# Optimization experiments

Hardware: AMD Instinct MI355X
Metric: run time of the kernel (lower is better)

Reference implementation:

```python
import jax, jax.numpy as jnp
import numpy as np

S_REF = 2        # number of reference images
C = 1024         # DINOv3 ViT-L channel dim
H = W = 64       # 1024 / patch16 feature resolution
SVD = 500        # positional subspace rank


def _l2norm(x, axis):
    return x / jnp.clip(jnp.linalg.norm(x, axis=axis, keepdims=True), 1e-12)


def setup_inputs() -> dict:
    key = jax.random.key(0)
    k1, k2, k3 = jax.random.split(key, 3)
    fmaps = jax.random.normal(k1, (1, S_REF + 1, C, H, W), jnp.float32)
    ref_masks = jax.random.randint(k2, (S_REF, H, W), 0, 2) > 0  # bool masks at feature res
    basis_raw = jax.random.normal(k3, (C, SVD), jnp.float32)
    basis, _ = jnp.linalg.qr(basis_raw)  # orthonormal positional basis, as SVD U would be
    return {"fmaps": fmaps, "ref_masks": ref_masks, "basis": basis}


def reference(fmaps, ref_masks, basis):
    S = ref_masks.shape[0]
    B, T, Cc, h, w = fmaps.shape

    # F.normalize(fmaps, p=2, dim=2)
    fn = _l2norm(fmaps, 2)
    feat_tgt = fn[0, S]  # (C,h,w) raw-normalized target feats

    # _debias_features: project onto orthogonal complement of positional subspace.
    # (I - U U^T) X computed as X - U (U^T X) to avoid a CxC matrix.
    X = fn.reshape(B * T, Cc, h * w)
    coef = jnp.einsum('ck,bcn->bkn', basis, X)          # (BT, SVD, hw)
    Xd = X - jnp.einsum('ck,bkn->bcn', basis, coef)     # (BT, C, hw)
    fd = _l2norm(Xd.reshape(B, T, Cc, h, w), 2)
    feat_refs_deb = fd[0, :S]   # (S,C,h,w)
    feat_tgt_deb = fd[0, S]     # (C,h,w)

    # Masked feature pooling -> per-reference prototype, then averaged + renormalized
    maskf = ref_masks.astype(fn.dtype)                                  # (S,h,w)
    counts = jnp.clip(maskf.sum(axis=(1, 2)), 1.0)                      # guard empty mask
    protos = jnp.einsum('schw,shw->sc', feat_refs_deb, maskf) / counts[:, None]
    ref_prototype = _l2norm(protos.mean(axis=0), 0)                     # (C,)

    # Dense ref->target cosine-similarity maps: einsum 'bchw,bcxy->bhwxy'
    sim = jnp.einsum('schw,cxy->shwxy', feat_refs_deb, feat_tgt_deb)    # (S,h,w,h,w)

    # Forward matching: target-vs-prototype similarity
    sim_fwd = jnp.einsum('cxy,c->xy', feat_tgt_deb, ref_prototype)      # (h,w)

    # Backward matching votes: for each target patch, argmax over ref patches,
    # vote if the best ref patch lies inside the reference mask.
    sim_t2r = sim.transpose(0, 3, 4, 1, 2).reshape(S, h * w, h * w)     # (S, tgt, ref)
    best_idx = jnp.argmax(sim_t2r, axis=2)                              # (S, hw)
    mask_flat = ref_masks.reshape(S, h * w)
    votes = jnp.take_along_axis(mask_flat, best_idx, axis=1).astype(jnp.int32)
    votes = votes.sum(axis=0).reshape(h, w)                             # (h,w) int32

    return sim, sim_fwd, votes
```

## Files before the change

kernel.cpp:

```cpp
#include <hip/hip_runtime.h>
#include <hip/hip_bf16.h>
#include <cfloat>

#define CH   1024
#define HW   4096
#define NSVD 500
#define TFR  3
#define SREF 2

typedef __attribute__((ext_vector_type(4))) float f32x4;
typedef __attribute__((ext_vector_type(4))) unsigned int u32x4;
typedef __attribute__((ext_vector_type(8))) short short8;


__device__ inline unsigned bfr(float x) {
  unsigned u = __float_as_uint(x);
  return (u + 0x7fffu + ((u >> 16) & 1u)) >> 16;
}
__device__ inline float lores(float x, unsigned h) {
  return x - __uint_as_float(h << 16);
}
__device__ inline float vlo(unsigned ph, unsigned pl) {
  return __uint_as_float(ph << 16) + __uint_as_float(pl << 16);
}
__device__ inline float vhi(unsigned ph, unsigned pl) {
  return __uint_as_float(ph & 0xFFFF0000u) + __uint_as_float(pl & 0xFFFF0000u);
}

__global__ __launch_bounds__(256) void normpack_k(const float* __restrict__ src,
                                                  unsigned* __restrict__ Gh,
                                                  unsigned* __restrict__ Gl,
                                                  int fbase) {
  int t = blockIdx.x >> 6;
  int n0 = (blockIdx.x & 63) * 64;
  int tid = threadIdx.x, nl = tid & 63, r = tid >> 6;
  const float* base = src + (size_t)t * CH * HW + n0 + nl;
  float s = 0.f;
  for (int c = r; c < CH; c += 4) {
    float v = base[(size_t)c * HW];
    s += v * v;
  }
  __shared__ float red[256];
  __shared__ float inv[64];
  red[tid] = s;
  __syncthreads();
  if (r == 0)
    inv[nl] = 1.0f / fmaxf(sqrtf(red[nl] + red[nl + 64] + red[nl + 128] + red[nl + 192]), 1e-12f);
  __syncthreads();

  int cg = (tid & 15) * 4;
  int n4 = n0 + cg;
  float4 w4;
  w4.x = inv[cg]; w4.y = inv[cg + 1]; w4.z = inv[cg + 2]; w4.w = inv[cg + 3];
  int gt = fbase + t;
  for (int kg = tid >> 4; kg < 128; kg += 16) {
    const float* s0 = src + ((size_t)t * CH + kg * 8) * HW + n4;
    unsigned oh[4][4], ol[4][4];
#pragma unroll
    for (int j = 0; j < 4; j++) {
      float4 va = *reinterpret_cast<const float4*>(s0 + (size_t)(2 * j) * HW);
      float4 vb = *reinterpret_cast<const float4*>(s0 + (size_t)(2 * j + 1) * HW);
      float a[4] = {va.x * w4.x, va.y * w4.y, va.z * w4.z, va.w * w4.w};
      float b[4] = {vb.x * w4.x, vb.y * w4.y, vb.z * w4.z, vb.w * w4.w};
#pragma unroll
      for (int cc = 0; cc < 4; cc++) {
        unsigned ha = bfr(a[cc]), hb = bfr(b[cc]);
        oh[cc][j] = ha | (hb << 16);
        ol[cc][j] = bfr(lores(a[cc], ha)) | (bfr(lores(b[cc], hb)) << 16);
      }
    }
    size_t vib = (((size_t)gt * 16 + (n4 >> 8)) * 128 + kg) * 256 + (n4 & 255);
#pragma unroll
    for (int cc = 0; cc < 4; cc++) {
      *reinterpret_cast<u32x4*>(Gh + (vib + cc) * 4) = *reinterpret_cast<u32x4*>(oh[cc]);
      *reinterpret_cast<u32x4*>(Gl + (vib + cc) * 4) = *reinterpret_cast<u32x4*>(ol[cc]);
    }
  }
}

__global__ __launch_bounds__(256) void scale_pack_k(const float* __restrict__ src,
                                                    const float* __restrict__ inv,
                                                    unsigned* __restrict__ Gh,
                                                    unsigned* __restrict__ Gl) {
  int gid = blockIdx.x * 256 + threadIdx.x;
  int kg = gid >> 12;
  int n = gid & 4095;
  const float* s0 = src + (size_t)(kg * 8) * HW + n;
  float w = inv[n];
  unsigned oh[4], ol[4];
#pragma unroll
  for (int j = 0; j < 4; j++) {
    float a = s0[(size_t)(2 * j) * HW] * w;
    float b = s0[(size_t)(2 * j + 1) * HW] * w;
    unsigned ha = bfr(a), hb = bfr(b);
    oh[j] = ha | (hb << 16);
    ol[j] = bfr(lores(a, ha)) | (bfr(lores(b, hb)) << 16);
  }
  size_t vi = (((size_t)(n >> 8)) * 128 + kg) * 256 + (n & 255);
  *reinterpret_cast<u32x4*>(Gh + vi * 4) = *reinterpret_cast<u32x4*>(oh);
  *reinterpret_cast<u32x4*>(Gl + vi * 4) = *reinterpret_cast<u32x4*>(ol);
}

__global__ __launch_bounds__(256) void bt_k(const float* __restrict__ bas,
                                            float* __restrict__ bt) {
  int c0 = blockIdx.x * 64;
  __shared__ float tile[64][129];
  int tid = threadIdx.x;
  for (int kc = 0; kc < 512; kc += 128) {
    for (int cr = tid >> 7; cr < 64; cr += 2) {
      int k = kc + (tid & 127);
      tile[cr][tid & 127] = (k < NSVD) ? bas[(size_t)(c0 + cr) * NSVD + k] : 0.f;
    }
    __syncthreads();
    for (int kr = tid >> 6; kr < 128; kr += 4)
      bt[(size_t)(kc + kr) * 1024 + c0 + (tid & 63)] = tile[tid & 63][kr];
    __syncthreads();
  }
}

__global__ __launch_bounds__(256) void proj_pack_k(const float* __restrict__ bt,
                                                   unsigned* __restrict__ Ah,
                                                   unsigned* __restrict__ Al) {
  int m0 = blockIdx.x * 64, n0 = blockIdx.y * 64;
  int tid = threadIdx.x;
  int tx = tid & 15, ty = tid >> 4;
  int lm = tid & 63, lk = tid >> 6;
  __shared__ float As[16][64];
  __shared__ float Bs[16][64];
  float acc[4][4] = {};
  for (int k0 = 0; k0 < 512; k0 += 16) {
#pragma unroll
    for (int i = 0; i < 4; i++) {
      int k = k0 + lk * 4 + i;
      As[lk * 4 + i][lm] = bt[(size_t)k * 1024 + m0 + lm];
      Bs[lk * 4 + i][lm] = bt[(size_t)k * 1024 + n0 + lm];
    }
    __syncthreads();
#pragma unroll
    for (int kk = 0; kk < 16; kk++) {
      float a[4], b[4];
#pragma unroll
      for (int i = 0; i < 4; i++) a[i] = As[kk][ty * 4 + i];
#pragma unroll
      for (int j = 0; j < 4; j++) b[j] = Bs[kk][tx * 4 + j];
#pragma unroll
      for (int i = 0; i < 4; i++)
#pragma unroll
        for (int j = 0; j < 4; j++) acc[i][j] += a[i] * b[j];
    }
    __syncthreads();
  }
#pragma unroll
  for (int jp = 0; jp < 2; jp++) {
    int r = n0 / 2 + tx * 2 + jp;
#pragma unroll
    for (int i = 0; i < 4; i++) {
      int c = m0 + ty * 4 + i;
      float va = ((c == 2 * r) ? 1.0f : 0.0f) - acc[i][2 * jp];
      float vb = ((c == 2 * r + 1) ? 1.0f : 0.0f) - acc[i][2 * jp + 1];
      unsigned ha = bfr(va), hb = bfr(vb);
      size_t vi = ((size_t)((c >> 8) * 128 + (r >> 2)) * 256 + (c & 255)) * 4 + (r & 3);
      Ah[vi] = ha | (hb << 16);
      Al[vi] = bfr(lores(va, ha)) | (bfr(lores(vb, hb)) << 16);
    }
  }
}

__global__ __launch_bounds__(256) void pack_basis_k(const float* __restrict__ bas,
                                                    unsigned* __restrict__ Ah,
                                                    unsigned* __restrict__ Al) {
  int r = blockIdx.x;
  for (int m = threadIdx.x; m < 512; m += 256) {
    float b0 = (m < NSVD) ? bas[(size_t)(2 * r) * NSVD + m] : 0.f;
    float b1 = (m < NSVD) ? bas[(size_t)(2 * r + 1) * NSVD + m] : 0.f;
    unsigned h0 = bfr(b0), h1 = bfr(b1);
    int c = 1024 + m;
    size_t vi = ((size_t)((c >> 8) * 128 + (r >> 2)) * 256 + (c & 255)) * 4 + (r & 3);
    Ah[vi] = h0 | (h1 << 16);
    Al[vi] = bfr(lores(b0, h0)) | (bfr(lores(b1, h1)) << 16);
  }
}

__global__ __launch_bounds__(256) void inv2_k(const float* __restrict__ pbuf,
                                              float* __restrict__ invc) {
  int i = blockIdx.x * 256 + threadIdx.x;
  int s = i >> 12, n = i & 4095;
  float s2 = 0.f;
  if (s < 2) {
#pragma unroll
    for (int j = 0; j < 4; j++) s2 += pbuf[(size_t)(s * 8 + j) * HW + n];
    s2 = sqrtf(fmaxf(1.0f - s2, 0.0f));
  } else {
#pragma unroll
    for (int j = 16; j < 24; j++) s2 += pbuf[(size_t)j * HW + n];
    s2 = sqrtf(s2);
  }
  invc[i] = 1.0f / fmaxf(s2, 1e-12f);
}

__global__ __launch_bounds__(256) void proto_k(const unsigned* __restrict__ Gh,
                                               const unsigned* __restrict__ Gl,
                                               const int* __restrict__ mask,
                                               const float* __restrict__ invc,
                                               float* __restrict__ protos,
                                               float* __restrict__ counts) {
  int s = blockIdx.x >> 7, kg = blockIdx.x & 127;
  int tid = threadIdx.x;
  const u32x4* Hv = (const u32x4*)Gh + (size_t)s * 524288;
  const u32x4* Lv = (const u32x4*)Gl + (size_t)s * 524288;
  float a[8] = {};
  int cnt = 0;
  for (int n = tid; n < HW; n += 256) {
    if (mask[s * HW + n]) {
      cnt++;
      float w = invc[s * HW + n];
      size_t vi = ((size_t)(n >> 8) * 128 + kg) * 256 + (n & 255);
      u32x4 h = Hv[vi], l = Lv[vi];
#pragma unroll
      for (int j = 0; j < 4; j++) {
        a[2 * j] += vlo(h[j], l[j]) * w;
        a[2 * j + 1] += vhi(h[j], l[j]) * w;
      }
    }
  }
  __shared__ float red[256];
  for (int e = 0; e < 8; e++) {
    red[tid] = a[e];
    __syncthreads();
    for (int o = 128; o > 0; o >>= 1) {
      if (tid < o) red[tid] += red[tid + o];
      __syncthreads();
    }
    if (tid == 0) protos[s * CH + kg * 8 + e] = red[0];
    __syncthreads();
  }
  if (kg == 0) {
    red[tid] = (float)cnt;
    __syncthreads();
    for (int o = 128; o > 0; o >>= 1) {
      if (tid < o) red[tid] += red[tid + o];
      __syncthreads();
    }
    if (tid == 0) counts[s] = fmaxf(red[0], 1.0f);
  }
}

__global__ __launch_bounds__(256) void protomv_k(const unsigned* __restrict__ Ah,
                                                 const unsigned* __restrict__ Al,
                                                 const float* __restrict__ protos,
                                                 float* __restrict__ part) {
  int s = blockIdx.x >> 2;
  int c = (blockIdx.x & 3) * 256 + threadIdx.x;
  int kc = blockIdx.y;
  __shared__ float w[128];
  if (threadIdx.x < 128) w[threadIdx.x] = protos[s * CH + kc * 128 + threadIdx.x];
  __syncthreads();
  float acc = 0.f;
  for (int rl = 0; rl < 64; rl++) {
    int r = kc * 64 + rl;
    size_t vi = ((size_t)((c >> 8) * 128 + (r >> 2)) * 256 + (c & 255)) * 4 + (r & 3);
    unsigned h = Ah[vi], l = Al[vi];
    acc += vlo(h, l) * w[2 * rl] + vhi(h, l) * w[2 * rl + 1];
  }
  part[kc * 2048 + s * CH + c] = acc;
}

__global__ __launch_bounds__(256) void protonorm_k(const float* __restrict__ part,
                                                   const float* __restrict__ counts,
                                                   float* __restrict__ proto) {
  int tid = threadIdx.x;
  __shared__ float sm[CH];
  __shared__ float red[256];
  float c0 = counts[0], c1 = counts[1];
  float ss = 0.f;
  for (int c = tid; c < CH; c += 256) {
    float p0 = 0.f, p1 = 0.f;
#pragma unroll
    for (int kc = 0; kc < 8; kc++) {
      p0 += part[kc * 2048 + c];
      p1 += part[kc * 2048 + CH + c];
    }
    float m = 0.5f * (p0 / c0 + p1 / c1);
    sm[c] = m;
    ss += m * m;
  }
  red[tid] = ss;
  __syncthreads();
  for (int o = 128; o > 0; o >>= 1) {
    if (tid < o) red[tid] += red[tid + o];
    __syncthreads();
  }
  __syncthreads();
  float inv = 1.0f / fmaxf(sqrtf(red[0]), 1e-12f);
  for (int c = tid; c < CH; c += 256) proto[c] = sm[c] * inv;
}

__global__ __launch_bounds__(256) void simfwd_k(const unsigned* __restrict__ Gh,
                                                const unsigned* __restrict__ Gl,
                                                const float* __restrict__ proto,
                                                float* __restrict__ out) {
  __shared__ float p[CH];
  __shared__ float red[256];
  int tid = threadIdx.x;
  for (int c = tid; c < CH; c += 256) p[c] = proto[c];
  __syncthreads();
  int nl = tid & 63, q = tid >> 6;
  int n = blockIdx.x * 64 + nl;
  const u32x4* Hv = (const u32x4*)Gh + (size_t)2 * 524288;
  const u32x4* Lv = (const u32x4*)Gl + (size_t)2 * 524288;
  float acc = 0.f;
  for (int kg = q * 32; kg < q * 32 + 32; kg++) {
    size_t vi = ((size_t)(n >> 8) * 128 + kg) * 256 + (n & 255);
    u32x4 h = Hv[vi], l = Lv[vi];
#pragma unroll
    for (int j = 0; j < 4; j++)
      acc += vlo(h[j], l[j]) * p[8 * kg + 2 * j] + vhi(h[j], l[j]) * p[8 * kg + 2 * j + 1];
  }
  red[tid] = acc;
  __syncthreads();
  if (q == 0) out[n] = red[nl] + red[nl + 64] + red[nl + 128] + red[nl + 192];
}

#define BM 128
#define BK 32

__device__ __forceinline__ short8 ldfrag(const unsigned* S, int loc, int q) {
  return *reinterpret_cast<const short8*>(&S[loc * 32 + ((q ^ (loc & 7)) << 2)]);
}

__global__ __launch_bounds__(256) void gemm3d_k(
    const unsigned* __restrict__ Ach, const unsigned* __restrict__ Acl,
    const unsigned* __restrict__ fh, const unsigned* __restrict__ fl,
    float* __restrict__ Xd, float* __restrict__ pbuf) {
  int bx = blockIdx.x, bz = blockIdx.z;
  bool isXd = (bz == 2);
  int m0 = bx * BM, cm0 = m0;
  int slot;
  if (isXd) {
    if (bx >= 8) return;
    slot = 16 + bx;
  } else {
    if (bx < 8) return;
    cm0 = (bx - 8) * BM;
    slot = bz * 8 + (bx - 8);
  }
  int n0 = blockIdx.y * BM;
  const u32x4* Ahv = (const u32x4*)Ach;
  const u32x4* Alv = (const u32x4*)Acl;
  const u32x4* Bhv = (const u32x4*)fh + (size_t)bz * 524288;
  const u32x4* Blv = (const u32x4*)fl + (size_t)bz * 524288;

  __shared__ u32x4 AsV[BM * 8];
  __shared__ u32x4 BsV[BM * 8];
  unsigned* As = (unsigned*)AsV;
  unsigned* Bs = (unsigned*)BsV;

  int tid = threadIdx.x;
  int lane = tid & 63, wave = tid >> 6;
  int wr = wave >> 1, wc = wave & 1;
  int sn = tid & 127, kq = tid >> 7;
  int fcol = lane & 15, l16 = lane >> 4;

  int colA = m0 + sn, colB = n0 + sn;
  size_t ia = (size_t)(colA >> 8) * 32768 + (colA & 255);
  size_t ib = (size_t)(colB >> 8) * 32768 + (colB & 255);

  f32x4 acc[4][4] = {};
  unsigned rah[8], ral[8], rbh[8], rbl[8];

#define LOADT(KT)                                                          \
  {                                                                        \
    int g0 = (KT) * 4 + kq * 2;                                            \
    *reinterpret_cast<u32x4*>(&rah[0]) = Ahv[ia + (size_t)g0 * 256];       \
    *reinterpret_cast<u32x4*>(&rah[4]) = Ahv[ia + (size_t)(g0 + 1) * 256]; \
    *reinterpret_cast<u32x4*>(&ral[0]) = Alv[ia + (size_t)g0 * 256];       \
    *reinterpret_cast<u32x4*>(&ral[4]) = Alv[ia + (size_t)(g0 + 1) * 256]; \
    *reinterpret_cast<u32x4*>(&rbh[0]) = Bhv[ib + (size_t)g0 * 256];       \
    *reinterpret_cast<u32x4*>(&rbh[4]) = Bhv[ib + (size_t)(g0 + 1) * 256]; \
    *reinterpret_cast<u32x4*>(&rbl[0]) = Blv[ib + (size_t)g0 * 256];       \
    *reinterpret_cast<u32x4*>(&rbl[4]) = Blv[ib + (size_t)(g0 + 1) * 256]; \
  }

  LOADT(0);

  for (int kt = 0; kt < CH / BK; ++kt) {
    __syncthreads();
    {
      int xa = sn & 7;
      int q0 = ((2 * kq) ^ xa) << 2, q1 = ((2 * kq + 1) ^ xa) << 2;
      int q2 = ((4 + 2 * kq) ^ xa) << 2, q3 = ((5 + 2 * kq) ^ xa) << 2;
      *reinterpret_cast<u32x4*>(&As[sn * 32 + q0]) = *reinterpret_cast<u32x4*>(&rah[0]);
      *reinterpret_cast<u32x4*>(&As[sn * 32 + q1]) = *reinterpret_cast<u32x4*>(&rah[4]);
      *reinterpret_cast<u32x4*>(&As[sn * 32 + q2]) = *reinterpret_cast<u32x4*>(&ral[0]);
      *reinterpret_cast<u32x4*>(&As[sn * 32 + q3]) = *reinterpret_cast<u32x4*>(&ral[4]);
      *reinterpret_cast<u32x4*>(&Bs[sn * 32 + q0]) = *reinterpret_cast<u32x4*>(&rbh[0]);
      *reinterpret_cast<u32x4*>(&Bs[sn * 32 + q1]) = *reinterpret_cast<u32x4*>(&rbh[4]);
      *reinterpret_cast<u32x4*>(&Bs[sn * 32 + q2]) = *reinterpret_cast<u32x4*>(&rbl[0]);
      *reinterpret_cast<u32x4*>(&Bs[sn * 32 + q3]) = *reinterpret_cast<u32x4*>(&rbl[4]);
    }
    __syncthreads();

    if (kt + 1 < CH / BK) LOADT(kt + 1);

    short8 bhf[4], blf[4];
#pragma unroll
    for (int nf = 0; nf < 4; nf++) {
      int nloc = wc * 64 + nf * 16 + fcol;
      bhf[nf] = ldfrag(Bs, nloc, l16);
      blf[nf] = ldfrag(Bs, nloc, 4 + l16);
    }
#pragma unroll
    for (int mf = 0; mf < 4; mf++) {
      int mloc = wr * 64 + mf * 16 + fcol;
      short8 ah = ldfrag(As, mloc, l16);
      short8 al = ldfrag(As, mloc, 4 + l16);
#pragma unroll
      for (int nf = 0; nf < 4; nf++) {
        acc[mf][nf] = __builtin_amdgcn_mfma_f32_16x16x32_bf16(ah, bhf[nf], acc[mf][nf], 0, 0, 0);
        acc[mf][nf] = __builtin_amdgcn_mfma_f32_16x16x32_bf16(ah, blf[nf], acc[mf][nf], 0, 0, 0);
        acc[mf][nf] = __builtin_amdgcn_mfma_f32_16x16x32_bf16(al, bhf[nf], acc[mf][nf], 0, 0, 0);
      }
    }
  }
#undef LOADT

  float s2p[4] = {0.f, 0.f, 0.f, 0.f};
  int rbase = l16 * 4;
#pragma unroll
  for (int mf = 0; mf < 4; mf++) {
    int mbase = cm0 + wr * 64 + mf * 16 + rbase;
#pragma unroll
    for (int r = 0; r < 4; r++) {
#pragma unroll
      for (int nf = 0; nf < 4; nf++) {
        float v = acc[mf][nf][r];
        s2p[nf] += v * v;
        if (isXd) {
          int n = n0 + wc * 64 + nf * 16 + fcol;
          Xd[(size_t)(mbase + r) * HW + n] = v;
        }
      }
    }
  }
#pragma unroll
  for (int nf = 0; nf < 4; nf++) {
    s2p[nf] += __shfl_xor(s2p[nf], 16, 64);
    s2p[nf] += __shfl_xor(s2p[nf], 32, 64);
  }
  __syncthreads();
  float* sred = (float*)As;
  if (wr == 0 && l16 == 0) {
#pragma unroll
    for (int nf = 0; nf < 4; nf++) sred[wc * 64 + nf * 16 + fcol] = s2p[nf];
  }
  __syncthreads();
  if (wr == 1 && l16 == 0) {
    float* dst = pbuf + (size_t)slot * HW + n0;
#pragma unroll
    for (int nf = 0; nf < 4; nf++) {
      int col = wc * 64 + nf * 16 + fcol;
      dst[col] = sred[col] + s2p[nf];
    }
  }
}

#define SIMG_NT 32

__global__ __launch_bounds__(512, 2) void simg_k(
    const unsigned* __restrict__ Gh, const unsigned* __restrict__ Gl,
    const float* __restrict__ invc, float* __restrict__ simout,
    unsigned long long* __restrict__ amg) {
  int orig = (blockIdx.z * 16 + blockIdx.y) * 16 + blockIdx.x;
  int lin = (orig & 7) * 64 + (orig >> 3);
  int z = lin >> 8, bx = (lin >> 4) & 15, by = lin & 15;

  const unsigned* Agh = Gh + (size_t)z * 2097152 + (size_t)bx * 131072;
  const unsigned* Agl = Gl + (size_t)z * 2097152 + (size_t)bx * 131072;
  const unsigned* Bgh = Gh + (size_t)2 * 2097152 + (size_t)by * 131072;
  const unsigned* Bgl = Gl + (size_t)2 * 2097152 + (size_t)by * 131072;

  int tid = threadIdx.x, ln = tid & 63, wv = tid >> 6;
  int wr = wv >> 2, wc = wv & 3;
  int fcol = ln & 15, l16 = ln >> 4;
  int aoff = l16 * 1024 + (wr * 128 + fcol) * 4;
  int boff = l16 * 1024 + (wc * 64 + fcol) * 4;

  f32x4 acc[8][4] = {};
  u32x4 ahr[8], alr[8], bhr[4], blr[4];

#define MFMA32(A, B)                                                          \
  _Pragma("unroll")                                                           \
  for (int mf = 0; mf < 8; mf++)                                              \
    _Pragma("unroll")                                                         \
    for (int nf = 0; nf < 4; nf++)                                            \
      acc[mf][nf] = __builtin_amdgcn_mfma_f32_16x16x32_bf16(                  \
          __builtin_bit_cast(short8, A[mf]), __builtin_bit_cast(short8, B[nf]), \
          acc[mf][nf], 0, 0, 0);

#pragma unroll
  for (int mf = 0; mf < 8; mf++)
    ahr[mf] = *reinterpret_cast<const u32x4*>(Agh + aoff + mf * 64);
#pragma unroll
  for (int nf = 0; nf < 4; nf++)
    blr[nf] = *reinterpret_cast<const u32x4*>(Bgl + boff + nf * 64);
#pragma unroll
  for (int nf = 0; nf < 4; nf++)
    bhr[nf] = *reinterpret_cast<const u32x4*>(Bgh + boff + nf * 64);
#pragma unroll
  for (int mf = 0; mf < 8; mf++)
    alr[mf] = *reinterpret_cast<const u32x4*>(Agl + aoff + mf * 64);

  for (int t = 0; t < SIMG_NT; ++t) {
    int nxt = (t + 1) * 4096;

    __builtin_amdgcn_s_setprio(1);
    MFMA32(ahr, bhr)
    __builtin_amdgcn_s_setprio(0);
    __builtin_amdgcn_sched_barrier(0);

    __builtin_amdgcn_s_setprio(1);
    MFMA32(ahr, blr)
    __builtin_amdgcn_s_setprio(0);
    __builtin_amdgcn_sched_barrier(0);
    if (t + 1 < SIMG_NT) {
#pragma unroll
      for (int mf = 0; mf < 8; mf++)
        ahr[mf] = *reinterpret_cast<const u32x4*>(Agh + nxt + aoff + mf * 64);
#pragma unroll
      for (int nf = 0; nf < 4; nf++)
        blr[nf] = *reinterpret_cast<const u32x4*>(Bgl + nxt + boff + nf * 64);
    }
    __builtin_amdgcn_sched_barrier(0);

    __builtin_amdgcn_s_setprio(1);
    MFMA32(alr, bhr)
    __builtin_amdgcn_s_setprio(0);
    __builtin_amdgcn_sched_barrier(0);
    if (t + 1 < SIMG_NT) {
#pragma unroll
      for (int nf = 0; nf < 4; nf++)
        bhr[nf] = *reinterpret_cast<const u32x4*>(Bgh + nxt + boff + nf * 64);
#pragma unroll
      for (int mf = 0; mf < 8; mf++)
        alr[mf] = *reinterpret_cast<const u32x4*>(Agl + nxt + aoff + mf * 64);
    }
    __builtin_amdgcn_sched_barrier(0);
  }
#undef MFMA32

  const float* rs = invc + (size_t)z * HW;
  float* C = simout + (size_t)z * HW * HW;
  unsigned long long* am = amg + (size_t)z * HW;
  int m0 = bx * 256, n0 = by * 256;
  int ncol[4];
#pragma unroll
  for (int nf = 0; nf < 4; nf++) ncol[nf] = n0 + wc * 64 + nf * 16 + fcol;
  float bv[4] = {-FLT_MAX, -FLT_MAX, -FLT_MAX, -FLT_MAX};
  int bi[4] = {0, 0, 0, 0};
#pragma unroll
  for (int mf = 0; mf < 8; mf++) {
    int mg = m0 + wr * 128 + mf * 16 + l16 * 4;
#pragma unroll
    for (int r = 0; r < 4; r++) {
      float sc = rs[mg + r];
#pragma unroll
      for (int nf = 0; nf < 4; nf++) {
        float val = acc[mf][nf][r] * sc;
        C[(size_t)(mg + r) * HW + ncol[nf]] = val;
        if (val > bv[nf]) { bv[nf] = val; bi[nf] = mg + r; }
      }
    }
  }
#pragma unroll
  for (int nf = 0; nf < 4; nf++) {
#pragma unroll
    for (int st = 16; st <= 32; st <<= 1) {
      float ov = __shfl_xor(bv[nf], st, 64);
      int oi = __shfl_xor(bi[nf], st, 64);
      if (ov > bv[nf] || (ov == bv[nf] && oi < bi[nf])) { bv[nf] = ov; bi[nf] = oi; }
    }
  }
  if (ln < 16) {
#pragma unroll
    for (int nf = 0; nf < 4; nf++) {
      unsigned b = __float_as_uint(bv[nf]);
      unsigned key = (b & 0x80000000u) ? ~b : (b | 0x80000000u);
      unsigned long long packed =
          ((unsigned long long)key << 32) | (unsigned)(~bi[nf]);
      atomicMax(am + ncol[nf], packed);
    }
  }
}

__global__ __launch_bounds__(256) void votes_k(const unsigned long long* __restrict__ am,
                                               const int* __restrict__ mask,
                                               float* __restrict__ out) {
  int xy = blockIdx.x * 256 + threadIdx.x;
  int vote = 0;
  for (int s = 0; s < SREF; s++) {
    unsigned long long p = am[(size_t)s * HW + xy];
    int bi = (int)(~(unsigned)p);
    vote += (mask[s * HW + bi] != 0);
  }
  out[xy] = (float)vote;
}

extern "C" void kernel_launch(void* const* d_in, const int* in_sizes, int n_in,
                              void* d_out, int out_size, void* d_ws, size_t ws_size,
                              hipStream_t stream) {
  const float* fmaps = (const float*)d_in[0];
  const int* mask = (const int*)d_in[1];
  const float* basis = (const float*)d_in[2];
  float* out = (float*)d_out;
  float* ws = (float*)d_ws;

  unsigned* fh = (unsigned*)ws;
  unsigned* fl = (unsigned*)(ws + 6291456);
  float* invc = ws + 12595200;
  float* protos = ws + 12607552;
  float* proto = ws + 12611648;
  unsigned long long* am = (unsigned long long*)(ws + 12612672);
  float* part = ws + 12629056;
  float* counts = ws + 12645440;

  float* sim = out;
  float* simfwd = out + 33554432;
  float* votes = out + 33558528;
  unsigned* Ach = (unsigned*)out;
  unsigned* Acl = (unsigned*)(out + 786432);
  float* bt = out + 1572864;
  float* Xd = out + 5767168;
  float* pbuf = out + 9961472;

  hipMemsetAsync(am, 0, (size_t)SREF * HW * sizeof(unsigned long long), stream);

  normpack_k<<<dim3(TFR * 64), 256, 0, stream>>>(fmaps, fh, fl, 0);

  bt_k<<<dim3(16), 256, 0, stream>>>(basis, bt);
  proj_pack_k<<<dim3(16, 16), 256, 0, stream>>>(bt, Ach, Acl);
  pack_basis_k<<<dim3(512), 256, 0, stream>>>(basis, Ach, Acl);

  gemm3d_k<<<dim3(12, 32, 3), 256, 0, stream>>>(Ach, Acl, fh, fl, Xd, pbuf);
  inv2_k<<<dim3(48), 256, 0, stream>>>(pbuf, invc);

  scale_pack_k<<<dim3(2048), 256, 0, stream>>>(Xd, invc + 2 * HW,
                                               fh + (size_t)2 * 2097152,
                                               fl + (size_t)2 * 2097152);

  proto_k<<<256, 256, 0, stream>>>(fh, fl, mask, invc, protos, counts);
  protomv_k<<<dim3(8, 8), 256, 0, stream>>>(Ach, Acl, protos, part);
  protonorm_k<<<1, 256, 0, stream>>>(part, counts, proto);

  simfwd_k<<<64, 256, 0, stream>>>(fh, fl, proto, simfwd);

  simg_k<<<dim3(16, 16, 2), 512, 0, stream>>>(fh, fl, invc, sim, am);

  votes_k<<<16, 256, 0, stream>>>(am, mask, votes);
}
```

Before: 450.9 us.

## Replace LDS-staged projection GEMM with register-direct MFMA kernel; split simfwd over K

The projection GEMM no longer stages tiles through shared memory. It now runs with 512-thread blocks on 128x256 tiles, loading MFMA fragments straight from global memory in their packed layout, with register double-buffering, s_setprio and sched_barrier interleaving. The block index is remapped to spread work across XCDs. The forward-similarity mat-vec is split four ways over channels into partial buffers, which the votes kernel sums to raise parallelism. This drops LDS traffic and barriers but depends on the packed layout matching fragment order and on L2 serving the repeated global loads.

```diff
diff --git a/kernel.cpp b/kernel.cpp
--- a/kernel.cpp
+++ b/kernel.cpp
@@ -298,137 +298,126 @@
 __global__ __launch_bounds__(256) void simfwd_k(const unsigned* __restrict__ Gh,
                                                 const unsigned* __restrict__ Gl,
                                                 const float* __restrict__ proto,
-                                                float* __restrict__ out) {
-  __shared__ float p[CH];
+                                                float* __restrict__ sfpart) {
+  int q = blockIdx.y;
+  __shared__ float p[256];
   __shared__ float red[256];
   int tid = threadIdx.x;
-  for (int c = tid; c < CH; c += 256) p[c] = proto[c];
-  __syncthreads();
-  int nl = tid & 63, q = tid >> 6;
+  p[tid] = proto[q * 256 + tid];
+  __syncthreads();
+  int nl = tid & 63, sub = tid >> 6;
   int n = blockIdx.x * 64 + nl;
   const u32x4* Hv = (const u32x4*)Gh + (size_t)2 * 524288;
   const u32x4* Lv = (const u32x4*)Gl + (size_t)2 * 524288;
   float acc = 0.f;
-  for (int kg = q * 32; kg < q * 32 + 32; kg++) {
+  for (int kg = q * 32 + sub * 8; kg < q * 32 + sub * 8 + 8; kg++) {
     size_t vi = ((size_t)(n >> 8) * 128 + kg) * 256 + (n & 255);
     u32x4 h = Hv[vi], l = Lv[vi];
+    int pb = (kg - q * 32) * 8;
 #pragma unroll
     for (int j = 0; j < 4; j++)
-      acc += vlo(h[j], l[j]) * p[8 * kg + 2 * j] + vhi(h[j], l[j]) * p[8 * kg + 2 * j + 1];
+      acc += vlo(h[j], l[j]) * p[pb + 2 * j] + vhi(h[j], l[j]) * p[pb + 2 * j + 1];
   }
   red[tid] = acc;
   __syncthreads();
-  if (q == 0) out[n] = red[nl] + red[nl + 64] + red[nl + 128] + red[nl + 192];
-}
-
-#define BM 128
-#define BK 32
-
-__device__ __forceinline__ short8 ldfrag(const unsigned* S, int loc, int q) {
-  return *reinterpret_cast<const short8*>(&S[loc * 32 + ((q ^ (loc & 7)) << 2)]);
-}
-
-__global__ __launch_bounds__(256) void gemm3d_k(
+  if (sub == 0)
+    sfpart[(size_t)q * HW + n] = red[nl] + red[nl + 64] + red[nl + 128] + red[nl + 192];
+}
+
+#define G3_NT 32
+
+__global__ __launch_bounds__(512, 2) void gemm3r_k(
     const unsigned* __restrict__ Ach, const unsigned* __restrict__ Acl,
     const unsigned* __restrict__ fh, const unsigned* __restrict__ fl,
     float* __restrict__ Xd, float* __restrict__ pbuf) {
-  int bx = blockIdx.x, bz = blockIdx.z;
-  bool isXd = (bz == 2);
-  int m0 = bx * BM, cm0 = m0;
-  int slot;
-  if (isXd) {
-    if (bx >= 8) return;
-    slot = 16 + bx;
-  } else {
-    if (bx < 8) return;
-    cm0 = (bx - 8) * BM;
-    slot = bz * 8 + (bx - 8);
-  }
-  int n0 = blockIdx.y * BM;
-  const u32x4* Ahv = (const u32x4*)Ach;
-  const u32x4* Alv = (const u32x4*)Acl;
-  const u32x4* Bhv = (const u32x4*)fh + (size_t)bz * 524288;
-  const u32x4* Blv = (const u32x4*)fl + (size_t)bz * 524288;
-
-  __shared__ u32x4 AsV[BM * 8];
-  __shared__ u32x4 BsV[BM * 8];
-  unsigned* As = (unsigned*)AsV;
-  unsigned* Bs = (unsigned*)BsV;
-
-  int tid = threadIdx.x;
-  int lane = tid & 63, wave = tid >> 6;
-  int wr = wave >> 1, wc = wave & 1;
-  int sn = tid & 127, kq = tid >> 7;
-  int fcol = lane & 15, l16 = lane >> 4;
-
-  int colA = m0 + sn, colB = n0 + sn;
-  size_t ia = (size_t)(colA >> 8) * 32768 + (colA & 255);
-  size_t ib = (size_t)(colB >> 8) * 32768 + (colB & 255);
+  int orig = blockIdx.x;
+  int lin = (orig & 7) * 32 + (orig >> 3);
+  int z, bx, by;
+  if (lin < 128) { z = lin >> 6; bx = (lin >> 4) & 3; by = lin & 15; }
+  else { int l2 = lin - 128; z = 2; bx = l2 >> 4; by = l2 & 15; }
+  bool isXd = (z == 2);
+  int acol0 = isXd ? bx * 128 : 1024 + bx * 128;
+  int acb = acol0 >> 8, aco = acol0 & 255;
+
+  const unsigned* Agh = Ach + (size_t)acb * 131072;
+  const unsigned* Agl = Acl + (size_t)acb * 131072;
+  const unsigned* Bgh = fh + (size_t)z * 2097152 + (size_t)by * 131072;
+  const unsigned* Bgl = fl + (size_t)z * 2097152 + (size_t)by * 131072;
+
+  int tid = threadIdx.x, ln = tid & 63, wv = tid >> 6;
+  int wr = wv >> 2, wc = wv & 3;
+  int fcol = ln & 15, l16 = ln >> 4;
+  int aoff = l16 * 1024 + (aco + wr * 64 + fcol) * 4;
+  int boff = l16 * 1024 + (wc * 64 + fcol) * 4;
 
   f32x4 acc[4][4] = {};
-  unsigned rah[8], ral[8], rbh[8], rbl[8];
-
-#define LOADT(KT)                                                          \
-  {                                                                        \
-    int g0 = (KT) * 4 + kq * 2;                                            \
-    *reinterpret_cast<u32x4*>(&rah[0]) = Ahv[ia + (size_t)g0 * 256];       \
-    *reinterpret_cast<u32x4*>(&rah[4]) = Ahv[ia + (size_t)(g0 + 1) * 256]; \
-    *reinterpret_cast<u32x4*>(&ral[0]) = Alv[ia + (size_t)g0 * 256];       \
-    *reinterpret_cast<u32x4*>(&ral[4]) = Alv[ia + (size_t)(g0 + 1) * 256]; \
-    *reinterpret_cast<u32x4*>(&rbh[0]) = Bhv[ib + (size_t)g0 * 256];       \
-    *reinterpret_cast<u32x4*>(&rbh[4]) = Bhv[ib + (size_t)(g0 + 1) * 256]; \
-    *reinterpret_cast<u32x4*>(&rbl[0]) = Blv[ib + (size_t)g0 * 256];       \
-    *reinterpret_cast<u32x4*>(&rbl[4]) = Blv[ib + (size_t)(g0 + 1) * 256]; \
-  }
-
-  LOADT(0);
-
-  for (int kt = 0; kt < CH / BK; ++kt) {
-    __syncthreads();
-    {
-      int xa = sn & 7;
-      int q0 = ((2 * kq) ^ xa) << 2, q1 = ((2 * kq + 1) ^ xa) << 2;
-      int q2 = ((4 + 2 * kq) ^ xa) << 2, q3 = ((5 + 2 * kq) ^ xa) << 2;
-      *reinterpret_cast<u32x4*>(&As[sn * 32 + q0]) = *reinterpret_cast<u32x4*>(&rah[0]);
-      *reinterpret_cast<u32x4*>(&As[sn * 32 + q1]) = *reinterpret_cast<u32x4*>(&rah[4]);
-      *reinterpret_cast<u32x4*>(&As[sn * 32 + q2]) = *reinterpret_cast<u32x4*>(&ral[0]);
-      *reinterpret_cast<u32x4*>(&As[sn * 32 + q3]) = *reinterpret_cast<u32x4*>(&ral[4]);
-      *reinterpret_cast<u32x4*>(&Bs[sn * 32 + q0]) = *reinterpret_cast<u32x4*>(&rbh[0]);
-      *reinterpret_cast<u32x4*>(&Bs[sn * 32 + q1]) = *reinterpret_cast<u32x4*>(&rbh[4]);
-      *reinterpret_cast<u32x4*>(&Bs[sn * 32 + q2]) = *reinterpret_cast<u32x4*>(&rbl[0]);
-      *reinterpret_cast<u32x4*>(&Bs[sn * 32 + q3]) = *reinterpret_cast<u32x4*>(&rbl[4]);
-    }
-    __syncthreads();
-
-    if (kt + 1 < CH / BK) LOADT(kt + 1);
-
-    short8 bhf[4], blf[4];
-#pragma unroll
-    for (int nf = 0; nf < 4; nf++) {
-      int nloc = wc * 64 + nf * 16 + fcol;
-      bhf[nf] = ldfrag(Bs, nloc, l16);
-      blf[nf] = ldfrag(Bs, nloc, 4 + l16);
-    }
-#pragma unroll
-    for (int mf = 0; mf < 4; mf++) {
-      int mloc = wr * 64 + mf * 16 + fcol;
-      short8 ah = ldfrag(As, mloc, l16);
-      short8 al = ldfrag(As, mloc, 4 + l16);
-#pragma unroll
-      for (int nf = 0; nf < 4; nf++) {
-        acc[mf][nf] = __builtin_amdgcn_mfma_f32_16x16x32_bf16(ah, bhf[nf], acc[mf][nf], 0, 0, 0);
-        acc[mf][nf] = __builtin_amdgcn_mfma_f32_16x16x32_bf16(ah, blf[nf], acc[mf][nf], 0, 0, 0);
-        acc[mf][nf] = __builtin_amdgcn_mfma_f32_16x16x32_bf16(al, bhf[nf], acc[mf][nf], 0, 0, 0);
-      }
-    }
-  }
-#undef LOADT
-
+  u32x4 ahr[4], alr[4], bhr[4], blr[4];
+
+#define MFMA16R(A, B)                                                         \
+  _Pragma("unroll")                                                           \
+  for (int mf = 0; mf < 4; mf++)                                              \
+    _Pragma("unroll")                                                         \
+    for (int nf = 0; nf < 4; nf++)                                            \
+      acc[mf][nf] = __builtin_amdgcn_mfma_f32_16x16x32_bf16(                  \
+          __builtin_bit_cast(short8, A[mf]), __builtin_bit_cast(short8, B[nf]), \
+          acc[mf][nf], 0, 0, 0);
+
+#pragma unroll
+  for (int mf = 0; mf < 4; mf++)
+    ahr[mf] = *reinterpret_cast<const u32x4*>(Agh + aoff + mf * 64);
+#pragma unroll
+  for (int nf = 0; nf < 4; nf++)
+    blr[nf] = *reinterpret_cast<const u32x4*>(Bgl + boff + nf * 64);
+#pragma unroll
+  for (int nf = 0; nf < 4; nf++)
+    bhr[nf] = *reinterpret_cast<const u32x4*>(Bgh + boff + nf * 64);
+#pragma unroll
+  for (int mf = 0; mf < 4; mf++)
+    alr[mf] = *reinterpret_cast<const u32x4*>(Agl + aoff + mf * 64);
+
+  for (int t = 0; t < G3_NT; ++t) {
+    int nxt = (t + 1) * 4096;
+
+    __builtin_amdgcn_s_setprio(1);
+    MFMA16R(ahr, bhr)
+    __builtin_amdgcn_s_setprio(0);
+    __builtin_amdgcn_sched_barrier(0);
+
+    __builtin_amdgcn_s_setprio(1);
+    MFMA16R(ahr, blr)
+    __builtin_amdgcn_s_setprio(0);
+    __builtin_amdgcn_sched_barrier(0);
+    if (t + 1 < G3_NT) {
+#pragma unroll
+      for (int mf = 0; mf < 4; mf++)
+        ahr[mf] = *reinterpret_cast<const u32x4*>(Agh + nxt + aoff + mf * 64);
+#pragma unroll
+      for (int nf = 0; nf < 4; nf++)
+        blr[nf] = *reinterpret_cast<const u32x4*>(Bgl + nxt + boff + nf * 64);
+    }
+    __builtin_amdgcn_sched_barrier(0);
+
+    __builtin_amdgcn_s_setprio(1);
+    MFMA16R(alr, bhr)
+    __builtin_amdgcn_s_setprio(0);
+    __builtin_amdgcn_sched_barrier(0);
+    if (t + 1 < G3_NT) {
+#pragma unroll
+      for (int nf = 0; nf < 4; nf++)
+        bhr[nf] = *reinterpret_cast<const u32x4*>(Bgh + nxt + boff + nf * 64);
+#pragma unroll
+      for (int mf = 0; mf < 4; mf++)
+        alr[mf] = *reinterpret_cast<const u32x4*>(Agl + nxt + aoff + mf * 64);
+    }
+    __builtin_amdgcn_sched_barrier(0);
+  }
+#undef MFMA16R
+
+  int n0 = by * 256;
   float s2p[4] = {0.f, 0.f, 0.f, 0.f};
-  int rbase = l16 * 4;
 #pragma unroll
   for (int mf = 0; mf < 4; mf++) {
-    int mbase = cm0 + wr * 64 + mf * 16 + rbase;
+    int mg = bx * 128 + wr * 64 + mf * 16 + l16 * 4;
 #pragma unroll
     for (int r = 0; r < 4; r++) {
 #pragma unroll
@@ -437,7 +426,7 @@
         s2p[nf] += v * v;
         if (isXd) {
           int n = n0 + wc * 64 + nf * 16 + fcol;
-          Xd[(size_t)(mbase + r) * HW + n] = v;
+          Xd[(size_t)(mg + r) * HW + n] = v;
         }
       }
     }
@@ -447,14 +436,14 @@
     s2p[nf] += __shfl_xor(s2p[nf], 16, 64);
     s2p[nf] += __shfl_xor(s2p[nf], 32, 64);
   }
-  __syncthreads();
-  float* sred = (float*)As;
+  __shared__ float sred[256];
   if (wr == 0 && l16 == 0) {
 #pragma unroll
     for (int nf = 0; nf < 4; nf++) sred[wc * 64 + nf * 16 + fcol] = s2p[nf];
   }
   __syncthreads();
   if (wr == 1 && l16 == 0) {
+    int slot = isXd ? 16 + bx : z * 8 + bx;
     float* dst = pbuf + (size_t)slot * HW + n0;
 #pragma unroll
     for (int nf = 0; nf < 4; nf++) {
@@ -594,8 +583,11 @@
 
 __global__ __launch_bounds__(256) void votes_k(const unsigned long long* __restrict__ am,
                                                const int* __restrict__ mask,
+                                               const float* __restrict__ sfpart,
+                                               float* __restrict__ simfwd,
                                                float* __restrict__ out) {
   int xy = blockIdx.x * 256 + threadIdx.x;
+  simfwd[xy] = ((sfpart[xy] + sfpart[HW + xy]) + sfpart[2 * HW + xy]) + sfpart[3 * HW + xy];
   int vote = 0;
   for (int s = 0; s < SREF; s++) {
     unsigned long long p = am[(size_t)s * HW + xy];
@@ -622,6 +614,7 @@
   unsigned long long* am = (unsigned long long*)(ws + 12612672);
   float* part = ws + 12629056;
   float* counts = ws + 12645440;
+  float* sfpart = ws + 12645504;
 
   float* sim = out;
   float* simfwd = out + 33554432;
@@ -640,7 +633,7 @@
   proj_pack_k<<<dim3(16, 16), 256, 0, stream>>>(bt, Ach, Acl);
   pack_basis_k<<<dim3(512), 256, 0, stream>>>(basis, Ach, Acl);
 
-  gemm3d_k<<<dim3(12, 32, 3), 256, 0, stream>>>(Ach, Acl, fh, fl, Xd, pbuf);
+  gemm3r_k<<<dim3(256), 512, 0, stream>>>(Ach, Acl, fh, fl, Xd, pbuf);
   inv2_k<<<dim3(48), 256, 0, stream>>>(pbuf, invc);
 
   scale_pack_k<<<dim3(2048), 256, 0, stream>>>(Xd, invc + 2 * HW,
@@ -651,9 +644,9 @@
   protomv_k<<<dim3(8, 8), 256, 0, stream>>>(Ach, Acl, protos, part);
   protonorm_k<<<1, 256, 0, stream>>>(part, counts, proto);
 
-  simfwd_k<<<64, 256, 0, stream>>>(fh, fl, proto, simfwd);
+  simfwd_k<<<dim3(64, 4), 256, 0, stream>>>(fh, fl, proto, sfpart);
 
   simg_k<<<dim3(16, 16, 2), 512, 0, stream>>>(fh, fl, invc, sim, am);
 
-  votes_k<<<16, 256, 0, stream>>>(am, mask, votes);
-}
+  votes_k<<<16, 256, 0, stream>>>(am, mask, sfpart, simfwd, votes);
+}
```

Result: faster. 408.5 us, median of 2 (-9.4%).
